# Kernel optimization log

Measured on AMD Instinct MI355X. Metric: run time of the kernel, lower is better.

Reference implementation:

```python
import jax, jax.numpy as jnp
import numpy as np

B, T, D = 4, 4096, 1024
EPS = 1e-5  # FusedRMSNormSwishGate default eps


def setup_inputs() -> dict:
    key = jax.random.key(0)
    ks = jax.random.split(key, 6)
    s = 1.0 / np.sqrt(D)
    return {
        "x": jax.random.normal(ks[0], (B, T, D), jnp.float32),
        "Wi": jax.random.normal(ks[1], (D, D), jnp.float32) * s,
        "Wf": jax.random.normal(ks[2], (D, D), jnp.float32) * s,
        "Wg": jax.random.normal(ks[3], (D, D), jnp.float32) * s,
        "Wo": jax.random.normal(ks[4], (D, D), jnp.float32) * s,
        "norm_w": jnp.ones((D,), jnp.float32),
    }


def _hgrn_scan(f, i):
    # h_t = f_t * h_{t-1} + i_t  (elementwise gated linear recurrence)
    # associative combine: (f1,i1) o (f2,i2) = (f1*f2, i1*f2 + i2)
    def combine(a, b):
        fa, ia = a
        fb, ib = b
        return fa * fb, ia * fb + ib

    _, h = jax.lax.associative_scan(combine, (f, i), axis=1)
    return h


def reference(x, Wi, Wf, Wg, Wo, norm_w):
    # projections
    i = x @ Wi.T                                  # [B,T,D]
    f = jax.nn.sigmoid(x @ Wf.T)                  # forget gate in (0,1)
    # swiglu(i, 1-f): silu on the value, gated by the input gate (1-f)
    inp = jax.nn.silu(i) * (1.0 - f)
    # hierarchically-gated linear recurrence (chunk/parallel scan form)
    h = _hgrn_scan(f, inp)                        # [B,T,D]
    # RMSNorm(h) * swish(g) output gate
    g = x @ Wg.T
    rms = h * jax.lax.rsqrt(jnp.mean(h * h, axis=-1, keepdims=True) + EPS)
    o = (rms * norm_w) * (g * jax.nn.sigmoid(g))
    return o @ Wo.T
```

## Files before the change

### kernel.cpp

```cpp
#include <hip/hip_runtime.h>
#include <hip/hip_bf16.h>

typedef unsigned short u16;
using bf16x8 = __bf16 __attribute__((ext_vector_type(8)));
using f32x4  = float  __attribute__((ext_vector_type(4)));

#define BB 4
#define TT 4096
#define DD 1024
#define MROWS (BB*TT)
#define CT 64
#define NC (TT/CT)

__device__ __forceinline__ float sigm(float x) { return 1.0f / (1.0f + __expf(-x)); }
__device__ __forceinline__ u16 f2bf(float f) {
    __hip_bfloat16 h = __float2bfloat16(f);
    return *reinterpret_cast<u16*>(&h);
}
__device__ __forceinline__ float bf2f(u16 u) { return __uint_as_float(((unsigned)u) << 16); }

__device__ __forceinline__ void async_cp16(const u16* g, u16* l) {
    __builtin_amdgcn_global_load_lds(
        (const __attribute__((address_space(1))) unsigned int*)g,
        (__attribute__((address_space(3))) unsigned int*)l, 16, 0, 0);
}

__global__ __launch_bounds__(256) void conv_x_kernel(const float* __restrict__ s,
                                                     u16* __restrict__ d) {
    size_t i = (size_t)blockIdx.x * 256 + threadIdx.x;
    float4 v = *(const float4*)(s + i * 4);
    ushort4 u;
    u.x = f2bf(v.x); u.y = f2bf(v.y); u.z = f2bf(v.z); u.w = f2bf(v.w);
    *(ushort4*)(d + i * 4) = u;
}

__global__ __launch_bounds__(256) void conv_w4_kernel(const float* __restrict__ w0,
                                                      const float* __restrict__ w1,
                                                      const float* __restrict__ w2,
                                                      const float* __restrict__ w3,
                                                      u16* __restrict__ dst) {
    int i = blockIdx.x * 256 + threadIdx.x;
    int sel = i >> 18;
    int off = i & 262143;
    const float* s = (sel == 0) ? w0 : (sel == 1) ? w1 : (sel == 2) ? w2 : w3;
    float4 v = *(const float4*)(s + (size_t)off * 4);
    ushort4 u;
    u.x = f2bf(v.x); u.y = f2bf(v.y); u.z = f2bf(v.z); u.w = f2bf(v.w);
    *(ushort4*)(dst + ((size_t)sel << 20) + (size_t)off * 4) = u;
}

#define BM 128
#define BN 128
#define BK 64

template <typename OutT>
__global__ __launch_bounds__(256, 2)
void gemm_bf16_bt(const u16* __restrict__ Ag, const u16* __restrict__ Bg, int K,
                  OutT* __restrict__ P0, OutT* __restrict__ P1, OutT* __restrict__ P2) {
    __shared__ u16 As[BM * BK];
    __shared__ u16 Bs[BN * BK];

    const int tid  = threadIdx.x;
    const int lane = tid & 63;
    const int wid  = tid >> 6;
    const int wm   = wid >> 1;
    const int wn   = wid & 1;
    const int lr   = lane & 15;
    const int lq   = lane >> 4;

    const long bM  = (long)blockIdx.y * BM;
    const long bN0 = (long)blockIdx.x * BN;

    const f32x4 zero = {0.f, 0.f, 0.f, 0.f};
    f32x4 acc[4][4];
#pragma unroll
    for (int i = 0; i < 4; i++)
#pragma unroll
        for (int j = 0; j < 4; j++) acc[i][j] = zero;

    for (int kt = 0; kt < K; kt += BK) {
        __syncthreads();
#pragma unroll
        for (int j = 0; j < 4; j++) {
            const int G  = j * 256 + tid;
            const int m  = G >> 3;
            const int p  = G & 7;
            const int gk = p ^ (m & 7);
            async_cp16(Ag + (bM + m) * K + kt + gk * 8, &As[G * 8]);
            async_cp16(Bg + (bN0 + m) * K + kt + gk * 8, &Bs[G * 8]);
        }
        __syncthreads();
#pragma unroll
        for (int kk = 0; kk < BK / 32; kk++) {
            bf16x8 av[4], bv[4];
#pragma unroll
            for (int f = 0; f < 4; f++) {
                const int am = wm * 64 + f * 16 + lr;
                const int ag = (kk * 4 + lq) ^ (am & 7);
                av[f] = *(const bf16x8*)(&As[am * 64 + ag * 8]);
                const int bn = wn * 64 + f * 16 + lr;
                const int bg = (kk * 4 + lq) ^ (bn & 7);
                bv[f] = *(const bf16x8*)(&Bs[bn * 64 + bg * 8]);
            }
#pragma unroll
            for (int i = 0; i < 4; i++)
#pragma unroll
                for (int j = 0; j < 4; j++)
                    acc[i][j] = __builtin_amdgcn_mfma_f32_16x16x32_bf16(av[i], bv[j],
                                                                        acc[i][j], 0, 0, 0);
        }
    }

    const int pl = (int)(bN0 >> 10);
    OutT* P = (pl == 0) ? P0 : ((pl == 1) ? P1 : P2);
    const int cn = (int)(bN0 & 1023);
#pragma unroll
    for (int i = 0; i < 4; i++) {
        const long m0 = bM + wm * 64 + i * 16 + lq * 4;
#pragma unroll
        for (int j = 0; j < 4; j++) {
            const int n = cn + wn * 64 + j * 16 + lr;
#pragma unroll
            for (int r = 0; r < 4; r++) {
                if constexpr (sizeof(OutT) == 2)
                    P[(m0 + r) * 1024 + n] = f2bf(acc[i][j][r]);
                else
                    P[(m0 + r) * 1024 + n] = acc[i][j][r];
            }
        }
    }
}

__global__ __launch_bounds__(256) void scan_pass1(const u16* __restrict__ ip,
                                                  const u16* __restrict__ fp,
                                                  float* __restrict__ Fc,
                                                  float* __restrict__ Ic) {
    const int tid = blockIdx.x * 256 + threadIdx.x;
    const int d = tid & 1023;
    const int c = (tid >> 10) & (NC - 1);
    const int b = tid >> 16;
    size_t base = ((size_t)(b * TT + c * CT) << 10) + d;
    float F = 1.f, I = 0.f;
#pragma unroll 8
    for (int t = 0; t < CT; t++) {
        float fv = bf2f(fp[base]);
        float iv = bf2f(ip[base]);
        base += DD;
        float f = sigm(fv);
        float v = iv * sigm(iv) * (1.f - f);
        I = fmaf(f, I, v);
        F *= f;
    }
    Fc[tid] = F;
    Ic[tid] = I;
}

__global__ __launch_bounds__(256) void scan_pass2(const float* __restrict__ Fc,
                                                  const float* __restrict__ Ic,
                                                  float* __restrict__ Hin) {
    const int tid = blockIdx.x * 256 + threadIdx.x;
    const int d = tid & 1023;
    const int b = tid >> 10;
    float H = 0.f;
    for (int c = 0; c < NC; c++) {
        const int idx = ((b * NC + c) << 10) + d;
        Hin[idx] = H;
        H = fmaf(Fc[idx], H, Ic[idx]);
    }
}

__global__ __launch_bounds__(256) void scan_pass3(const u16* __restrict__ ip,
                                                  const u16* __restrict__ fp,
                                                  const float* __restrict__ Hin,
                                                  u16* __restrict__ hout) {
    const int tid = blockIdx.x * 256 + threadIdx.x;
    const int d = tid & 1023;
    const int c = (tid >> 10) & (NC - 1);
    const int b = tid >> 16;
    size_t base = ((size_t)(b * TT + c * CT) << 10) + d;
    float h = Hin[tid];
#pragma unroll 8
    for (int t = 0; t < CT; t++) {
        float fv = bf2f(fp[base]);
        float iv = bf2f(ip[base]);
        float f = sigm(fv);
        float v = iv * sigm(iv) * (1.f - f);
        h = fmaf(f, h, v);
        hout[base] = f2bf(h);
        base += DD;
    }
}

__global__ __launch_bounds__(256) void rmsnorm_gate(const u16* hin,
                                                    const u16* __restrict__ g,
                                                    const float* __restrict__ w,
                                                    u16* oout) {
    const int row = blockIdx.x;
    const int t = threadIdx.x;
    const size_t base = ((size_t)row << 10) + t * 4;
    ushort4 hu = *(const ushort4*)(hin + base);
    float h0 = bf2f(hu.x), h1 = bf2f(hu.y), h2 = bf2f(hu.z), h3 = bf2f(hu.w);
    float ss = h0 * h0 + h1 * h1 + h2 * h2 + h3 * h3;
#pragma unroll
    for (int o = 32; o > 0; o >>= 1) ss += __shfl_down(ss, o);
    __shared__ float red[4];
    if ((t & 63) == 0) red[t >> 6] = ss;
    __syncthreads();
    const float tot = red[0] + red[1] + red[2] + red[3];
    const float rms = rsqrtf(tot * (1.f / 1024.f) + 1e-5f);
    ushort4 gu = *(const ushort4*)(g + base);
    float g0 = bf2f(gu.x), g1 = bf2f(gu.y), g2 = bf2f(gu.z), g3 = bf2f(gu.w);
    float4 wv = *(const float4*)(w + (size_t)t * 4);
    ushort4 ou;
    ou.x = f2bf(h0 * rms * wv.x * g0 * sigm(g0));
    ou.y = f2bf(h1 * rms * wv.y * g1 * sigm(g1));
    ou.z = f2bf(h2 * rms * wv.z * g2 * sigm(g2));
    ou.w = f2bf(h3 * rms * wv.w * g3 * sigm(g3));
    *(ushort4*)(oout + base) = ou;
}

extern "C" void kernel_launch(void* const* d_in, const int* in_sizes, int n_in,
                              void* d_out, int out_size, void* d_ws, size_t ws_size,
                              hipStream_t stream) {
    const float* x  = (const float*)d_in[0];
    const float* Wi = (const float*)d_in[1];
    const float* Wf = (const float*)d_in[2];
    const float* Wg = (const float*)d_in[3];
    const float* Wo = (const float*)d_in[4];
    const float* nw = (const float*)d_in[5];
    float* out = (float*)d_out;

    const size_t MB = 1ull << 20;
    char* ws = (char*)d_ws;
    u16*   xo  = (u16*)(ws);
    u16*   Wb  = (u16*)(ws + 32 * MB);
    u16*   Pi  = (u16*)(ws + 40 * MB);
    u16*   Pf  = (u16*)(ws + 72 * MB);
    float* Fc  = (float*)(ws + 104 * MB);
    float* Ic  = Fc + BB * NC * DD;
    float* Hin = Ic + BB * NC * DD;
    u16*   g   = (u16*)d_out;

    conv_x_kernel<<<16384, 256, 0, stream>>>(x, xo);
    conv_w4_kernel<<<4096, 256, 0, stream>>>(Wi, Wf, Wg, Wo, Wb);
    gemm_bf16_bt<u16><<<dim3(24, 128), 256, 0, stream>>>(xo, Wb, 1024, Pi, Pf, g);
    scan_pass1<<<1024, 256, 0, stream>>>(Pi, Pf, Fc, Ic);
    scan_pass2<<<16, 256, 0, stream>>>(Fc, Ic, Hin);
    scan_pass3<<<1024, 256, 0, stream>>>(Pi, Pf, Hin, xo);
    rmsnorm_gate<<<16384, 256, 0, stream>>>(xo, g, nw, xo);
    gemm_bf16_bt<float><<<dim3(8, 128), 256, 0, stream>>>(xo, Wb + 3ull * 1024 * 1024, 1024,
                                                          out, out, out);
}
```

Measured before the change: 368.7 us.

## Vectorize scan passes 1/3 and parallelize chunk-prefix pass with wave shuffles

Scan passes 1 and 3 now handle four adjacent channels per thread, using 8-byte ushort4 loads and stores and float4 writes for the chunk summaries. That cuts the block count from 1024 to 256. Pass 2 replaces the serial 64-step loop over chunks (only 16 blocks) with a wave-level Hillis-Steele scan over chunks via shuffles, launching 1024 blocks. Wider loads raise memory efficiency, but fewer threads in passes 1 and 3 lower the parallelism available to hide the latency of the sequential time loop.

```diff
diff --git a/kernel.cpp b/kernel.cpp
--- a/kernel.cpp
+++ b/kernel.cpp
@@ -136,37 +136,58 @@
                                                   float* __restrict__ Fc,
                                                   float* __restrict__ Ic) {
     const int tid = blockIdx.x * 256 + threadIdx.x;
-    const int d = tid & 1023;
-    const int c = (tid >> 10) & (NC - 1);
-    const int b = tid >> 16;
-    size_t base = ((size_t)(b * TT + c * CT) << 10) + d;
-    float F = 1.f, I = 0.f;
+    const int d4  = tid & 255;
+    const int c   = (tid >> 8) & (NC - 1);
+    const int b   = tid >> 14;
+    size_t base = ((size_t)(b * TT + c * CT) << 10) + (size_t)d4 * 4;
+    float F[4] = {1.f, 1.f, 1.f, 1.f};
+    float I[4] = {0.f, 0.f, 0.f, 0.f};
 #pragma unroll 8
     for (int t = 0; t < CT; t++) {
-        float fv = bf2f(fp[base]);
-        float iv = bf2f(ip[base]);
+        ushort4 fu = *(const ushort4*)(fp + base);
+        ushort4 iu = *(const ushort4*)(ip + base);
         base += DD;
-        float f = sigm(fv);
-        float v = iv * sigm(iv) * (1.f - f);
-        I = fmaf(f, I, v);
-        F *= f;
-    }
-    Fc[tid] = F;
-    Ic[tid] = I;
+        const u16 fa[4] = {fu.x, fu.y, fu.z, fu.w};
+        const u16 ia[4] = {iu.x, iu.y, iu.z, iu.w};
+#pragma unroll
+        for (int j = 0; j < 4; j++) {
+            float f  = sigm(bf2f(fa[j]));
+            float iv = bf2f(ia[j]);
+            float v  = iv * sigm(iv) * (1.f - f);
+            I[j] = fmaf(f, I[j], v);
+            F[j] *= f;
+        }
+    }
+    const size_t o = (((size_t)(b * NC + c)) << 10) + (size_t)d4 * 4;
+    float4 vF = {F[0], F[1], F[2], F[3]};
+    float4 vI = {I[0], I[1], I[2], I[3]};
+    *(float4*)(Fc + o) = vF;
+    *(float4*)(Ic + o) = vI;
 }
 
 __global__ __launch_bounds__(256) void scan_pass2(const float* __restrict__ Fc,
                                                   const float* __restrict__ Ic,
                                                   float* __restrict__ Hin) {
-    const int tid = blockIdx.x * 256 + threadIdx.x;
-    const int d = tid & 1023;
-    const int b = tid >> 10;
-    float H = 0.f;
-    for (int c = 0; c < NC; c++) {
-        const int idx = ((b * NC + c) << 10) + d;
-        Hin[idx] = H;
-        H = fmaf(Fc[idx], H, Ic[idx]);
-    }
+    const int gtid = blockIdx.x * 256 + threadIdx.x;
+    const int lane = gtid & 63;
+    const int w    = gtid >> 6;
+    const int b    = w >> 10;
+    const int d    = w & 1023;
+    const int idx  = ((b * NC + lane) << 10) + d;
+    float F = Fc[idx];
+    float I = Ic[idx];
+#pragma unroll
+    for (int s = 1; s < 64; s <<= 1) {
+        float Fp = __shfl_up(F, s, 64);
+        float Ip = __shfl_up(I, s, 64);
+        if (lane >= s) {
+            I = fmaf(Ip, F, I);
+            F *= Fp;
+        }
+    }
+    float Hex = __shfl_up(I, 1, 64);
+    if (lane == 0) Hex = 0.f;
+    Hin[idx] = Hex;
 }
 
 __global__ __launch_bounds__(256) void scan_pass3(const u16* __restrict__ ip,
@@ -174,19 +195,31 @@
                                                   const float* __restrict__ Hin,
                                                   u16* __restrict__ hout) {
     const int tid = blockIdx.x * 256 + threadIdx.x;
-    const int d = tid & 1023;
-    const int c = (tid >> 10) & (NC - 1);
-    const int b = tid >> 16;
-    size_t base = ((size_t)(b * TT + c * CT) << 10) + d;
-    float h = Hin[tid];
+    const int d4  = tid & 255;
+    const int c   = (tid >> 8) & (NC - 1);
+    const int b   = tid >> 14;
+    size_t base = ((size_t)(b * TT + c * CT) << 10) + (size_t)d4 * 4;
+    const size_t o = (((size_t)(b * NC + c)) << 10) + (size_t)d4 * 4;
+    float4 hv = *(const float4*)(Hin + o);
+    float h[4] = {hv.x, hv.y, hv.z, hv.w};
 #pragma unroll 8
     for (int t = 0; t < CT; t++) {
-        float fv = bf2f(fp[base]);
-        float iv = bf2f(ip[base]);
-        float f = sigm(fv);
-        float v = iv * sigm(iv) * (1.f - f);
-        h = fmaf(f, h, v);
-        hout[base] = f2bf(h);
+        ushort4 fu = *(const ushort4*)(fp + base);
+        ushort4 iu = *(const ushort4*)(ip + base);
+        const u16 fa[4] = {fu.x, fu.y, fu.z, fu.w};
+        const u16 ia[4] = {iu.x, iu.y, iu.z, iu.w};
+        ushort4 ou;
+        u16 oa[4];
+#pragma unroll
+        for (int j = 0; j < 4; j++) {
+            float f  = sigm(bf2f(fa[j]));
+            float iv = bf2f(ia[j]);
+            float v  = iv * sigm(iv) * (1.f - f);
+            h[j] = fmaf(f, h[j], v);
+            oa[j] = f2bf(h[j]);
+        }
+        ou.x = oa[0]; ou.y = oa[1]; ou.z = oa[2]; ou.w = oa[3];
+        *(ushort4*)(hout + base) = ou;
         base += DD;
     }
 }
@@ -244,9 +277,9 @@
     conv_x_kernel<<<16384, 256, 0, stream>>>(x, xo);
     conv_w4_kernel<<<4096, 256, 0, stream>>>(Wi, Wf, Wg, Wo, Wb);
     gemm_bf16_bt<u16><<<dim3(24, 128), 256, 0, stream>>>(xo, Wb, 1024, Pi, Pf, g);
-    scan_pass1<<<1024, 256, 0, stream>>>(Pi, Pf, Fc, Ic);
-    scan_pass2<<<16, 256, 0, stream>>>(Fc, Ic, Hin);
-    scan_pass3<<<1024, 256, 0, stream>>>(Pi, Pf, Hin, xo);
+    scan_pass1<<<256, 256, 0, stream>>>(Pi, Pf, Fc, Ic);
+    scan_pass2<<<1024, 256, 0, stream>>>(Fc, Ic, Hin);
+    scan_pass3<<<256, 256, 0, stream>>>(Pi, Pf, Hin, xo);
     rmsnorm_gate<<<16384, 256, 0, stream>>>(xo, g, nw, xo);
     gemm_bf16_bt<float><<<dim3(8, 128), 256, 0, stream>>>(xo, Wb + 3ull * 1024 * 1024, 1024,
                                                           out, out, out);
```

Result: slower. 382.6 us (+3.8%).
